# Optimization experiments

Hardware: AMD Instinct MI355X
Metric: run time of the kernel (lower is better)

Reference implementation:

```python
import jax, jax.numpy as jnp
import numpy as np

B, T, D, H = 1, 2048, 1024, 16
HS = D // H  # 64
FF = 4 * D   # 4096
EPS = 1e-6


def rmsnorm(x, w):
    xf = x.astype(jnp.float32)
    n = xf * jax.lax.rsqrt(jnp.mean(xf * xf, axis=-1, keepdims=True) + EPS)
    return n.astype(x.dtype) * w


def setup_inputs() -> dict:
    key = jax.random.key(0)
    ks = jax.random.split(key, 9)
    s = 0.02
    return {
        "x": jax.random.normal(ks[0], (B, T, D), jnp.float32),
        "Wq": jax.random.normal(ks[1], (H, D, HS), jnp.float32) * s,
        "Wk": jax.random.normal(ks[2], (H, D, HS), jnp.float32) * s,
        "Wv": jax.random.normal(ks[3], (H, D, HS), jnp.float32) * s,
        "Wproj": jax.random.normal(ks[4], (H * HS, D), jnp.float32) * s,
        "bproj": jnp.zeros((D,), jnp.float32),
        "W1": jax.random.normal(ks[5], (D, FF), jnp.float32) * s,
        "W2": jax.random.normal(ks[6], (FF, D), jnp.float32) * s,
        "g1": jnp.ones((D,), jnp.float32),
        "g2": jnp.ones((D,), jnp.float32),
    }


def reference(x, Wq, Wk, Wv, Wproj, bproj, W1, W2, g1, g2):
    # --- self attention on RMSNorm(x) ---
    xn = rmsnorm(x, g1)                                   # [B,T,D]
    q = jnp.einsum('btd,hds->bhts', xn, Wq)               # [B,H,T,hs]
    k = jnp.einsum('btd,hds->bhts', xn, Wk)
    v = jnp.einsum('btd,hds->bhts', xn, Wv)
    scale = HS ** -0.5
    wei = jnp.einsum('bhts,bhus->bhtu', q, k) * scale     # [B,H,T,T]
    causal = jnp.tril(jnp.ones((T, T), bool))
    wei = jnp.where(causal, wei, -jnp.inf)
    wei = jax.nn.softmax(wei, axis=-1)
    attn = jnp.einsum('bhtu,bhus->bhts', wei, v)          # [B,H,T,hs]
    attn = attn.transpose(0, 2, 1, 3).reshape(B, T, H * HS)
    sa = attn @ Wproj + bproj                             # [B,T,D]
    x = x + sa
    # --- SiLU FFN on RMSNorm(x) ---
    xn2 = rmsnorm(x, g2)
    h = jax.nn.silu(xn2 @ W1)                             # [B,T,4D]
    x = x + h @ W2
    return x
```

## Files before the change

### kernel.cpp

```cpp
#include <hip/hip_runtime.h>

typedef unsigned short u16;
typedef unsigned int u32;
typedef __attribute__((ext_vector_type(4))) float f32x4;
typedef __attribute__((ext_vector_type(8))) __bf16 bf16x8;

#define T_SEQ 2048
#define DMODEL 1024
#define NHEAD 16
#define HEADS 64
#define FFDIM 4096
#define MNQ 2097152l

__device__ __forceinline__ u16 f2bf(float f) {
  u32 u = __builtin_bit_cast(u32, f);
  u = u + 0x7FFFu + ((u >> 16) & 1u);
  return (u16)(u >> 16);
}
__device__ __forceinline__ float bf2f(u16 h) {
  u32 u = ((u32)h) << 16;
  return __builtin_bit_cast(float, u);
}
__device__ __forceinline__ void gload_lds16(const u16* g, u16* l) {
  __builtin_amdgcn_global_load_lds(
      (const __attribute__((address_space(1))) u32*)g,
      (__attribute__((address_space(3))) u32*)l, 16, 0, 0);
}

__global__ __launch_bounds__(256) void prep_k(
    const float* __restrict__ Wq, const float* __restrict__ Wk,
    const float* __restrict__ Wv, const float* __restrict__ Wproj,
    const float* __restrict__ W1, const float* __restrict__ W2,
    const float* __restrict__ x, const float* __restrict__ g1,
    u16* __restrict__ QKVwT, u16* __restrict__ WprojT,
    u16* __restrict__ W1T, u16* __restrict__ W2T, u16* __restrict__ xn1) {
  __shared__ u16 tile[64 * 66];
  __shared__ float wsum[4];
  int bid = blockIdx.x;
  int tid = threadIdx.x;
  if (bid >= 3072) {
    int row = bid - 3072;
    const float4* xr = (const float4*)(x + (long)row * DMODEL);
    float4 v = xr[tid];
    float ss = v.x * v.x + v.y * v.y + v.z * v.z + v.w * v.w;
#pragma unroll
    for (int off = 32; off >= 1; off >>= 1) ss += __shfl_xor(ss, off, 64);
    if ((tid & 63) == 0) wsum[tid >> 6] = ss;
    __syncthreads();
    float tot = wsum[0] + wsum[1] + wsum[2] + wsum[3];
    float rms = rsqrtf(tot * (1.0f / DMODEL) + 1e-6f);
    float4 gv = ((const float4*)g1)[tid];
    ushort4 o4 = make_ushort4(f2bf(v.x * rms * gv.x), f2bf(v.y * rms * gv.y),
                              f2bf(v.z * rms * gv.z), f2bf(v.w * rms * gv.w));
    ((ushort4*)(xn1 + (long)row * DMODEL))[tid] = o4;
    return;
  }
  const float* in;
  u16* out;
  long ldin, ldout;
  int r0, c0;
  if (bid < 768) {
    int z = bid >> 4, xi = bid & 15;
    int wsel = z >> 4, h = z & 15;
    in = (wsel == 0 ? Wq : (wsel == 1 ? Wk : Wv)) + (long)h * 65536;
    out = QKVwT + (long)wsel * 1048576 + (long)h * 65536;
    ldin = 64; ldout = 1024;
    r0 = xi * 64; c0 = 0;
  } else if (bid < 1024) {
    int b = bid - 768;
    in = Wproj; out = WprojT; ldin = 1024; ldout = 1024;
    r0 = (b >> 4) * 64; c0 = (b & 15) * 64;
  } else if (bid < 2048) {
    int b = bid - 1024;
    in = W1; out = W1T; ldin = 4096; ldout = 1024;
    r0 = (b & 15) * 64; c0 = (b >> 4) * 64;
  } else {
    int b = bid - 2048;
    in = W2; out = W2T; ldin = 1024; ldout = 4096;
    r0 = (b >> 4) * 64; c0 = (b & 15) * 64;
  }
#pragma unroll
  for (int p = 0; p < 16; ++p) {
    int idx = p * 256 + tid;
    int r = idx >> 6, c = idx & 63;
    tile[c * 66 + r] = f2bf(in[(long)(r0 + r) * ldin + c0 + c]);
  }
  __syncthreads();
#pragma unroll
  for (int p = 0; p < 16; ++p) {
    int idx = p * 256 + tid;
    int c = idx >> 6, r = idx & 63;
    out[(long)(c0 + c) * ldout + r0 + r] = tile[c * 66 + r];
  }
}

__global__ __launch_bounds__(256) void proj_rms_k(
    const u16* __restrict__ part, const float* __restrict__ bias,
    const float* __restrict__ resid, const float* __restrict__ g,
    float* __restrict__ x1, u16* __restrict__ xn2) {
  int row = blockIdx.x;
  int tid = threadIdx.x;
  long i = (long)row * DMODEL + tid * 4;
  float4 r = *(const float4*)(resid + i);
  float4 bi = *(const float4*)(bias + tid * 4);
  float4 v;
  v.x = r.x + bi.x; v.y = r.y + bi.y; v.z = r.z + bi.z; v.w = r.w + bi.w;
#pragma unroll
  for (int z = 0; z < 2; ++z) {
    ushort4 a = *(const ushort4*)(part + z * MNQ + i);
    v.x += bf2f(a.x); v.y += bf2f(a.y); v.z += bf2f(a.z); v.w += bf2f(a.w);
  }
  *(float4*)(x1 + i) = v;
  float ss = v.x * v.x + v.y * v.y + v.z * v.z + v.w * v.w;
#pragma unroll
  for (int off = 32; off >= 1; off >>= 1) ss += __shfl_xor(ss, off, 64);
  __shared__ float wsum[4];
  if ((tid & 63) == 0) wsum[tid >> 6] = ss;
  __syncthreads();
  float tot = wsum[0] + wsum[1] + wsum[2] + wsum[3];
  float rms = rsqrtf(tot * (1.0f / DMODEL) + 1e-6f);
  float4 gv = ((const float4*)g)[tid];
  ushort4 o4 = make_ushort4(f2bf(v.x * rms * gv.x), f2bf(v.y * rms * gv.y),
                            f2bf(v.z * rms * gv.z), f2bf(v.w * rms * gv.w));
  ((ushort4*)(xn2 + (long)row * DMODEL))[tid] = o4;
}

template <int EPI, int MODE>
__global__ __launch_bounds__(256, 3) void gemm_bt_k(
    const u16* __restrict__ A, const u16* __restrict__ Bt, int N, int K, int kc,
    u16* __restrict__ out16, u16* __restrict__ vt, u16* __restrict__ part) {
  __shared__ __align__(16) u16 As[3][128 * 32];
  __shared__ __align__(16) u16 Bs[3][128 * 32];
  int tid = threadIdx.x;
  int w = tid >> 6, lane = tid & 63;
  int quad = lane >> 4, l15 = lane & 15;
  int wr = w >> 1, wc = w & 1;

  int bid = blockIdx.x;
  int xcd = bid & 7, s = bid >> 3;
  int nn = N >> 7;
  int bx, by, kz;
  if (MODE == 0) {
    int nl = nn >> 3;
    by = xcd * nl + s % nl;
    int r = s / nl;
    bx = r & 15;
    kz = r >> 4;
  } else {
    bx = xcd * 2 + (s & 1);
    int r = s >> 1;
    by = r % nn;
    kz = r / nn;
  }
  int m0 = bx * 128, n0 = by * 128;

  f32x4 acc[4][4] = {};

  int lr = lane >> 2, lc = (lane & 3) * 8;
  const u16* Ak = A + (long)(m0 + w * 32 + lr) * K + lc + (long)kz * kc;
  const u16* A2k = Ak + (long)16 * K;
  const u16* Bk = Bt + (long)(n0 + w * 32 + lr) * K + lc + (long)kz * kc;
  const u16* B2k = Bk + (long)16 * K;
  u16* Aw[3] = {As[0] + w * 1024, As[1] + w * 1024, As[2] + w * 1024};
  u16* Bw[3] = {Bs[0] + w * 1024, Bs[1] + w * 1024, Bs[2] + w * 1024};

  int niter = kc >> 5;

  gload_lds16(Ak, Aw[0]);
  gload_lds16(A2k, Aw[0] + 512);
  gload_lds16(Bk, Bw[0]);
  gload_lds16(B2k, Bw[0] + 512);
  gload_lds16(Ak + 32, Aw[1]);
  gload_lds16(A2k + 32, Aw[1] + 512);
  gload_lds16(Bk + 32, Bw[1]);
  gload_lds16(B2k + 32, Bw[1] + 512);

  int cb = 0;
  for (int k = 0; k < niter; ++k) {
    if (k + 2 < niter) {
      asm volatile("s_waitcnt vmcnt(4)\n\ts_barrier" ::: "memory");
      int pb = (cb == 0) ? 2 : cb - 1;
      int off = (k + 2) * 32;
      gload_lds16(Ak + off, Aw[pb]);
      gload_lds16(A2k + off, Aw[pb] + 512);
      gload_lds16(Bk + off, Bw[pb]);
      gload_lds16(B2k + off, Bw[pb] + 512);
    } else {
      asm volatile("s_waitcnt vmcnt(0)\n\ts_barrier" ::: "memory");
    }
    const u16* Ab = As[cb];
    const u16* Bb = Bs[cb];
    bf16x8 af[4], bfr[4];
#pragma unroll
    for (int mt = 0; mt < 4; ++mt)
      af[mt] = *(const bf16x8*)(Ab + (wr * 64 + mt * 16 + l15) * 32 + quad * 8);
#pragma unroll
    for (int nt = 0; nt < 4; ++nt)
      bfr[nt] = *(const bf16x8*)(Bb + (wc * 64 + nt * 16 + l15) * 32 + quad * 8);
#pragma unroll
    for (int mt = 0; mt < 4; ++mt)
#pragma unroll
      for (int nt = 0; nt < 4; ++nt)
        acc[mt][nt] = __builtin_amdgcn_mfma_f32_16x16x32_bf16(
            af[mt], bfr[nt], acc[mt][nt], 0, 0, 0);
    cb = (cb == 2) ? 0 : cb + 1;
  }

  bool vblock = (EPI == 0) && (vt != nullptr) && (n0 >= 2048);
  u16* pb = nullptr;
  if (EPI == 4) pb = part + (long)kz * MNQ;
#pragma unroll
  for (int mt = 0; mt < 4; ++mt)
#pragma unroll
    for (int nt = 0; nt < 4; ++nt) {
      int col = n0 + wc * 64 + nt * 16 + l15;
      if (EPI == 0 && vblock) {
        int sc = col - 2048;
        int row0 = m0 + wr * 64 + mt * 16 + quad * 4;
        ushort4 pk = make_ushort4(f2bf(acc[mt][nt][0]), f2bf(acc[mt][nt][1]),
                                  f2bf(acc[mt][nt][2]), f2bf(acc[mt][nt][3]));
        *(ushort4*)(vt + (long)sc * 2048 + row0) = pk;
        continue;
      }
#pragma unroll
      for (int r = 0; r < 4; ++r) {
        int row = m0 + wr * 64 + mt * 16 + quad * 4 + r;
        long idx = (long)row * N + col;
        float v = acc[mt][nt][r];
        if (EPI == 0) {
          out16[idx] = f2bf(v);
        } else if (EPI == 2) {
          out16[idx] = f2bf(v / (1.0f + __expf(-v)));
        } else if (EPI == 4) {
          pb[idx] = f2bf(v);
        }
      }
    }
}

__global__ __launch_bounds__(256) void reduce_ffn2_k(
    const u16* __restrict__ part, const float* __restrict__ resid,
    float* __restrict__ out) {
  long i = ((long)blockIdx.x * 256 + threadIdx.x) * 4;
  float4 r = *(const float4*)(resid + i);
  float4 o = r;
#pragma unroll
  for (int z = 0; z < 4; ++z) {
    ushort4 a = *(const ushort4*)(part + z * MNQ + i);
    o.x += bf2f(a.x); o.y += bf2f(a.y); o.z += bf2f(a.z); o.w += bf2f(a.w);
  }
  *(float4*)(out + i) = o;
}

#define LSTR 72
__global__ __launch_bounds__(256) void attn_part_k(const u16* __restrict__ QKV,
                                                   const u16* __restrict__ Vt,
                                                   u16* __restrict__ Opart,
                                                   float* __restrict__ lpart) {
  __shared__ __align__(16) u16 Qs[64 * LSTR];
  __shared__ __align__(16) u16 Ks[64 * LSTR];
  __shared__ __align__(16) u16 Vs[64 * LSTR];
  __shared__ float lbuf[64];

  int tid = threadIdx.x;
  int w = tid >> 6, lane = tid & 63;
  int quad = lane >> 4, l15 = lane & 15;

  int bid = blockIdx.x;
  int xcd = bid & 7, sg = bid >> 3;
  int h = xcd * 2 + (sg & 1);
  int p = sg >> 1;

  int bx = 0, acc0 = 0;
  while (true) {
    int n = (bx >> 3) + 1;
    if (p < acc0 + n) break;
    acc0 += n;
    ++bx;
  }
  int c = p - acc0;
  int t0 = bx * 64;
  int jstart = c * 8;
  int jend = min(jstart + 8, bx + 1);

#pragma unroll
  for (int pp = 0; pp < 2; ++pp) {
    int idx = pp * 256 + tid;
    int row = idx >> 3, cc = idx & 7;
    *(uint4*)(Qs + row * LSTR + cc * 8) =
        *(const uint4*)(QKV + (long)(t0 + row) * 3072 + h * 64 + cc * 8);
  }
  __syncthreads();
  bf16x8 aq[2];
#pragma unroll
  for (int ks = 0; ks < 2; ++ks)
    aq[ks] = *(const bf16x8*)(Qs + (w * 16 + l15) * LSTR + ks * 32 + quad * 8);

  f32x4 oacc[4] = {};
  float lsum = 0.f;
  int qg = t0 + w * 16 + l15;

  u16* PsW = Qs + w * (16 * LSTR);

  for (int j = jstart; j < jend; ++j) {
    __syncthreads();
#pragma unroll
    for (int pp = 0; pp < 2; ++pp) {
      int idx = pp * 256 + tid;
      int row = idx >> 3, cc = idx & 7;
      *(uint4*)(Ks + row * LSTR + cc * 8) =
          *(const uint4*)(QKV + (long)(j * 64 + row) * 3072 + 1024 + h * 64 + cc * 8);
      *(uint4*)(Vs + row * LSTR + cc * 8) =
          *(const uint4*)(Vt + (long)h * (64 * 2048) + (long)row * 2048 + j * 64 + cc * 8);
    }
    __syncthreads();

    f32x4 sacc[4] = {};
#pragma unroll
    for (int ks = 0; ks < 2; ++ks)
#pragma unroll
      for (int ut = 0; ut < 4; ++ut) {
        bf16x8 kf = *(const bf16x8*)(Ks + (ut * 16 + l15) * LSTR + ks * 32 + quad * 8);
        sacc[ut] = __builtin_amdgcn_mfma_f32_16x16x32_bf16(kf, aq[ks], sacc[ut], 0, 0, 0);
      }

    bool boundary = (j == bx);
#pragma unroll
    for (int ut = 0; ut < 4; ++ut) {
      float pv[4];
#pragma unroll
      for (int r = 0; r < 4; ++r) {
        float v = exp2f(sacc[ut][r] * 0.18033688f);
        if (boundary) {
          int u = j * 64 + ut * 16 + quad * 4 + r;
          if (u > qg) v = 0.f;
        }
        pv[r] = v;
        lsum += v;
      }
      ushort4 pk = make_ushort4(f2bf(pv[0]), f2bf(pv[1]), f2bf(pv[2]), f2bf(pv[3]));
      *(ushort4*)(PsW + l15 * LSTR + ut * 16 + quad * 4) = pk;
    }
    asm volatile("s_waitcnt lgkmcnt(0)" ::: "memory");
#pragma unroll
    for (int ks = 0; ks < 2; ++ks) {
      bf16x8 pf = *(const bf16x8*)(PsW + l15 * LSTR + ks * 32 + quad * 8);
#pragma unroll
      for (int ct = 0; ct < 4; ++ct) {
        bf16x8 vf = *(const bf16x8*)(Vs + (ct * 16 + l15) * LSTR + ks * 32 + quad * 8);
        oacc[ct] = __builtin_amdgcn_mfma_f32_16x16x32_bf16(pf, vf, oacc[ct], 0, 0, 0);
      }
    }
  }

  lsum += __shfl_xor(lsum, 16, 64);
  lsum += __shfl_xor(lsum, 32, 64);
  if (quad == 0) lbuf[w * 16 + l15] = 1.0f / lsum;
  asm volatile("s_waitcnt lgkmcnt(0)" ::: "memory");

  long slot = (long)p * 16 + h;
  float inv[4];
#pragma unroll
  for (int r = 0; r < 4; ++r) inv[r] = lbuf[w * 16 + quad * 4 + r];
  u16* Ob = Opart + slot * 4096;
#pragma unroll
  for (int ct = 0; ct < 4; ++ct)
#pragma unroll
    for (int r = 0; r < 4; ++r)
      Ob[(w * 16 + quad * 4 + r) * 64 + ct * 16 + l15] = f2bf(oacc[ct][r] * inv[r]);
  if (quad == 0) lpart[slot * 64 + w * 16 + l15] = lsum;
}

__global__ __launch_bounds__(256) void attn_combine_k(
    const u16* __restrict__ Opart, const float* __restrict__ lpart,
    u16* __restrict__ out) {
  int bx = blockIdx.x, h = blockIdx.y;
  int g = bx >> 3;
  int p0 = 4 * g * (g + 1) + (bx - 8 * g) * (g + 1);
  int nc = g + 1;
  int tid = threadIdx.x;
  int row = tid >> 2, c4 = (tid & 3) * 16;

  float lv[4];
  float wsum = 0.f;
  for (int cidx = 0; cidx < nc; ++cidx) {
    long slot = (long)(p0 + cidx) * 16 + h;
    lv[cidx] = lpart[slot * 64 + row];
    wsum += lv[cidx];
  }
  float rinv = 1.0f / wsum;

  float o[16];
#pragma unroll
  for (int i = 0; i < 16; ++i) o[i] = 0.f;
  for (int cidx = 0; cidx < nc; ++cidx) {
    float wc = lv[cidx] * rinv;
    const u16* Ob = Opart + ((long)(p0 + cidx) * 16 + h) * 4096 + row * 64 + c4;
    bf16x8 a = *(const bf16x8*)Ob;
    bf16x8 b = *(const bf16x8*)(Ob + 8);
#pragma unroll
    for (int i = 0; i < 8; ++i) {
      o[i] += wc * (float)a[i];
      o[8 + i] += wc * (float)b[i];
    }
  }
  u16 ob[16];
#pragma unroll
  for (int i = 0; i < 16; ++i) ob[i] = f2bf(o[i]);
  u16* op = out + (long)(bx * 64 + row) * 1024 + h * 64 + c4;
  *(uint4*)op = *(uint4*)ob;
  *(uint4*)(op + 8) = *(uint4*)(ob + 8);
}

extern "C" void kernel_launch(void* const* d_in, const int* in_sizes, int n_in,
                              void* d_out, int out_size, void* d_ws, size_t ws_size,
                              hipStream_t stream) {
  const float* x     = (const float*)d_in[0];
  const float* Wq    = (const float*)d_in[1];
  const float* Wk    = (const float*)d_in[2];
  const float* Wv    = (const float*)d_in[3];
  const float* Wproj = (const float*)d_in[4];
  const float* bproj = (const float*)d_in[5];
  const float* W1    = (const float*)d_in[6];
  const float* W2    = (const float*)d_in[7];
  const float* g1    = (const float*)d_in[8];
  const float* g2    = (const float*)d_in[9];

  char* ws = (char*)d_ws;
  u16* QKVwT  = (u16*)(ws);
  u16* WprojT = (u16*)(ws + (6ul << 20));
  u16* W1T    = (u16*)(ws + (8ul << 20));
  u16* W2T    = (u16*)(ws + (16ul << 20));
  u16* xn1    = (u16*)(ws + (24ul << 20));
  u16* QKVb   = (u16*)(ws + (28ul << 20));
  u16* VtB    = (u16*)(ws + (40ul << 20));
  u16* attn   = (u16*)(ws + (44ul << 20));
  float* x1   = (float*)(ws + (48ul << 20));
  u16* xn2    = (u16*)(ws + (56ul << 20));
  u16* hbuf   = (u16*)(ws + (60ul << 20));
  u16* Opart    = (u16*)(ws + (48ul << 20));
  float* lpart  = (float*)(ws + (58ul << 20));
  u16* projp    = (u16*)(ws + (28ul << 20));
  u16* ffn2p    = (u16*)(ws + (28ul << 20));
  if (ws_size < (76ul << 20)) return;

  dim3 blk(256);

  prep_k<<<dim3(5120), blk, 0, stream>>>(
      Wq, Wk, Wv, Wproj, W1, W2, x, g1, QKVwT, WprojT, W1T, W2T, xn1);
  gemm_bt_k<0, 0><<<dim3(384), blk, 0, stream>>>(
      xn1, QKVwT, 3072, 1024, 1024, QKVb, VtB, nullptr);
  attn_part_k<<<dim3(1280), blk, 0, stream>>>(QKVb, VtB, Opart, lpart);
  attn_combine_k<<<dim3(32, 16), blk, 0, stream>>>(Opart, lpart, attn);
  gemm_bt_k<4, 0><<<dim3(256), blk, 0, stream>>>(
      attn, WprojT, 1024, 1024, 512, nullptr, nullptr, projp);
  proj_rms_k<<<dim3(2048), blk, 0, stream>>>(projp, bproj, x, g2, x1, xn2);
  gemm_bt_k<2, 0><<<dim3(512), blk, 0, stream>>>(
      xn2, W1T, 4096, 1024, 1024, hbuf, nullptr, nullptr);
  gemm_bt_k<4, 1><<<dim3(512), blk, 0, stream>>>(
      hbuf, W2T, 1024, 4096, 1024, nullptr, nullptr, ffn2p);
  reduce_ffn2_k<<<dim3(2048), blk, 0, stream>>>(ffn2p, x1, (float*)d_out);
}
```

Baseline: 254.9 us.

## Template GEMM K-loop count, split FFN2 over 8 K chunks, write single-chunk attention directly

The GEMM kernel now takes its iteration count as a template parameter so the K loop fully unrolls and buffer indices become compile-time constants. The FFN2 GEMM is split over eight K chunks instead of four, doubling the grid to 1024 blocks, with partials written to two buffers and summed in the reduce kernel. Attention blocks for the first query tiles, which have only one KV chunk, now write normalized output straight into the attention buffer, and the combine kernel skips those tiles. The cost is more partial-sum traffic for FFN2 and larger unrolled code.

```diff
diff --git a/kernel.cpp b/kernel.cpp
--- a/kernel.cpp
+++ b/kernel.cpp
@@ -125,12 +125,15 @@
   ((ushort4*)(xn2 + (long)row * DMODEL))[tid] = o4;
 }
 
-template <int EPI, int MODE>
+template <int EPI, int MODE, int NITER>
 __global__ __launch_bounds__(256, 3) void gemm_bt_k(
-    const u16* __restrict__ A, const u16* __restrict__ Bt, int N, int K, int kc,
-    u16* __restrict__ out16, u16* __restrict__ vt, u16* __restrict__ part) {
+    const u16* __restrict__ A, const u16* __restrict__ Bt, int N,
+    u16* __restrict__ out16, u16* __restrict__ vt,
+    u16* __restrict__ p0, u16* __restrict__ p1) {
   __shared__ __align__(16) u16 As[3][128 * 32];
   __shared__ __align__(16) u16 Bs[3][128 * 32];
+  const int K = 1024 * ((EPI == 4 && MODE == 1) ? 4 : 1);
+  const int kc = NITER * 32;
   int tid = threadIdx.x;
   int w = tid >> 6, lane = tid & 63;
   int quad = lane >> 4, l15 = lane & 15;
@@ -161,30 +164,27 @@
   const u16* A2k = Ak + (long)16 * K;
   const u16* Bk = Bt + (long)(n0 + w * 32 + lr) * K + lc + (long)kz * kc;
   const u16* B2k = Bk + (long)16 * K;
-  u16* Aw[3] = {As[0] + w * 1024, As[1] + w * 1024, As[2] + w * 1024};
-  u16* Bw[3] = {Bs[0] + w * 1024, Bs[1] + w * 1024, Bs[2] + w * 1024};
-
-  int niter = kc >> 5;
-
-  gload_lds16(Ak, Aw[0]);
-  gload_lds16(A2k, Aw[0] + 512);
-  gload_lds16(Bk, Bw[0]);
-  gload_lds16(B2k, Bw[0] + 512);
-  gload_lds16(Ak + 32, Aw[1]);
-  gload_lds16(A2k + 32, Aw[1] + 512);
-  gload_lds16(Bk + 32, Bw[1]);
-  gload_lds16(B2k + 32, Bw[1] + 512);
-
-  int cb = 0;
-  for (int k = 0; k < niter; ++k) {
-    if (k + 2 < niter) {
+
+  gload_lds16(Ak, As[0] + w * 1024);
+  gload_lds16(A2k, As[0] + w * 1024 + 512);
+  gload_lds16(Bk, Bs[0] + w * 1024);
+  gload_lds16(B2k, Bs[0] + w * 1024 + 512);
+  gload_lds16(Ak + 32, As[1] + w * 1024);
+  gload_lds16(A2k + 32, As[1] + w * 1024 + 512);
+  gload_lds16(Bk + 32, Bs[1] + w * 1024);
+  gload_lds16(B2k + 32, Bs[1] + w * 1024 + 512);
+
+#pragma unroll
+  for (int k = 0; k < NITER; ++k) {
+    const int cb = k % 3;
+    if (k + 2 < NITER) {
       asm volatile("s_waitcnt vmcnt(4)\n\ts_barrier" ::: "memory");
-      int pb = (cb == 0) ? 2 : cb - 1;
-      int off = (k + 2) * 32;
-      gload_lds16(Ak + off, Aw[pb]);
-      gload_lds16(A2k + off, Aw[pb] + 512);
-      gload_lds16(Bk + off, Bw[pb]);
-      gload_lds16(B2k + off, Bw[pb] + 512);
+      const int pb = (k + 2) % 3;
+      const int off = (k + 2) * 32;
+      gload_lds16(Ak + off, As[pb] + w * 1024);
+      gload_lds16(A2k + off, As[pb] + w * 1024 + 512);
+      gload_lds16(Bk + off, Bs[pb] + w * 1024);
+      gload_lds16(B2k + off, Bs[pb] + w * 1024 + 512);
     } else {
       asm volatile("s_waitcnt vmcnt(0)\n\ts_barrier" ::: "memory");
     }
@@ -203,12 +203,11 @@
       for (int nt = 0; nt < 4; ++nt)
         acc[mt][nt] = __builtin_amdgcn_mfma_f32_16x16x32_bf16(
             af[mt], bfr[nt], acc[mt][nt], 0, 0, 0);
-    cb = (cb == 2) ? 0 : cb + 1;
   }
 
   bool vblock = (EPI == 0) && (vt != nullptr) && (n0 >= 2048);
   u16* pb = nullptr;
-  if (EPI == 4) pb = part + (long)kz * MNQ;
+  if (EPI == 4) pb = (kz < 4 ? p0 : p1) + (long)(kz & 3) * MNQ;
 #pragma unroll
   for (int mt = 0; mt < 4; ++mt)
 #pragma unroll
@@ -239,15 +238,19 @@
 }
 
 __global__ __launch_bounds__(256) void reduce_ffn2_k(
-    const u16* __restrict__ part, const float* __restrict__ resid,
-    float* __restrict__ out) {
+    const u16* __restrict__ p0, const u16* __restrict__ p1,
+    const float* __restrict__ resid, float* __restrict__ out) {
   long i = ((long)blockIdx.x * 256 + threadIdx.x) * 4;
   float4 r = *(const float4*)(resid + i);
   float4 o = r;
 #pragma unroll
   for (int z = 0; z < 4; ++z) {
-    ushort4 a = *(const ushort4*)(part + z * MNQ + i);
-    o.x += bf2f(a.x); o.y += bf2f(a.y); o.z += bf2f(a.z); o.w += bf2f(a.w);
+    ushort4 a = *(const ushort4*)(p0 + z * MNQ + i);
+    ushort4 b = *(const ushort4*)(p1 + z * MNQ + i);
+    o.x += bf2f(a.x) + bf2f(b.x);
+    o.y += bf2f(a.y) + bf2f(b.y);
+    o.z += bf2f(a.z) + bf2f(b.z);
+    o.w += bf2f(a.w) + bf2f(b.w);
   }
   *(float4*)(out + i) = o;
 }
@@ -256,7 +259,8 @@
 __global__ __launch_bounds__(256) void attn_part_k(const u16* __restrict__ QKV,
                                                    const u16* __restrict__ Vt,
                                                    u16* __restrict__ Opart,
-                                                   float* __restrict__ lpart) {
+                                                   float* __restrict__ lpart,
+                                                   u16* __restrict__ attn) {
   __shared__ __align__(16) u16 Qs[64 * LSTR];
   __shared__ __align__(16) u16 Ks[64 * LSTR];
   __shared__ __align__(16) u16 Vs[64 * LSTR];
@@ -358,10 +362,20 @@
   if (quad == 0) lbuf[w * 16 + l15] = 1.0f / lsum;
   asm volatile("s_waitcnt lgkmcnt(0)" ::: "memory");
 
+  float inv[4];
+#pragma unroll
+  for (int r = 0; r < 4; ++r) inv[r] = lbuf[w * 16 + quad * 4 + r];
+
+  if (bx < 8) {
+#pragma unroll
+    for (int ct = 0; ct < 4; ++ct)
+#pragma unroll
+      for (int r = 0; r < 4; ++r)
+        attn[(long)(t0 + w * 16 + quad * 4 + r) * 1024 + h * 64 + ct * 16 + l15] =
+            f2bf(oacc[ct][r] * inv[r]);
+    return;
+  }
   long slot = (long)p * 16 + h;
-  float inv[4];
-#pragma unroll
-  for (int r = 0; r < 4; ++r) inv[r] = lbuf[w * 16 + quad * 4 + r];
   u16* Ob = Opart + slot * 4096;
 #pragma unroll
   for (int ct = 0; ct < 4; ++ct)
@@ -374,7 +388,7 @@
 __global__ __launch_bounds__(256) void attn_combine_k(
     const u16* __restrict__ Opart, const float* __restrict__ lpart,
     u16* __restrict__ out) {
-  int bx = blockIdx.x, h = blockIdx.y;
+  int bx = blockIdx.x + 8, h = blockIdx.y;
   int g = bx >> 3;
   int p0 = 4 * g * (g + 1) + (bx - 8 * g) * (g + 1);
   int nc = g + 1;
@@ -441,23 +455,24 @@
   u16* Opart    = (u16*)(ws + (48ul << 20));
   float* lpart  = (float*)(ws + (58ul << 20));
   u16* projp    = (u16*)(ws + (28ul << 20));
-  u16* ffn2p    = (u16*)(ws + (28ul << 20));
+  u16* ffn2pA   = (u16*)(ws + (28ul << 20));
+  u16* ffn2pB   = (u16*)(ws);
   if (ws_size < (76ul << 20)) return;
 
   dim3 blk(256);
 
   prep_k<<<dim3(5120), blk, 0, stream>>>(
       Wq, Wk, Wv, Wproj, W1, W2, x, g1, QKVwT, WprojT, W1T, W2T, xn1);
-  gemm_bt_k<0, 0><<<dim3(384), blk, 0, stream>>>(
-      xn1, QKVwT, 3072, 1024, 1024, QKVb, VtB, nullptr);
-  attn_part_k<<<dim3(1280), blk, 0, stream>>>(QKVb, VtB, Opart, lpart);
-  attn_combine_k<<<dim3(32, 16), blk, 0, stream>>>(Opart, lpart, attn);
-  gemm_bt_k<4, 0><<<dim3(256), blk, 0, stream>>>(
-      attn, WprojT, 1024, 1024, 512, nullptr, nullptr, projp);
+  gemm_bt_k<0, 0, 32><<<dim3(384), blk, 0, stream>>>(
+      xn1, QKVwT, 3072, QKVb, VtB, nullptr, nullptr);
+  attn_part_k<<<dim3(1280), blk, 0, stream>>>(QKVb, VtB, Opart, lpart, attn);
+  attn_combine_k<<<dim3(24, 16), blk, 0, stream>>>(Opart, lpart, attn);
+  gemm_bt_k<4, 0, 16><<<dim3(256), blk, 0, stream>>>(
+      attn, WprojT, 1024, nullptr, nullptr, projp, nullptr);
   proj_rms_k<<<dim3(2048), blk, 0, stream>>>(projp, bproj, x, g2, x1, xn2);
-  gemm_bt_k<2, 0><<<dim3(512), blk, 0, stream>>>(
-      xn2, W1T, 4096, 1024, 1024, hbuf, nullptr, nullptr);
-  gemm_bt_k<4, 1><<<dim3(512), blk, 0, stream>>>(
-      hbuf, W2T, 1024, 4096, 1024, nullptr, nullptr, ffn2p);
-  reduce_ffn2_k<<<dim3(2048), blk, 0, stream>>>(ffn2p, x1, (float*)d_out);
-}
+  gemm_bt_k<2, 0, 32><<<dim3(512), blk, 0, stream>>>(
+      xn2, W1T, 4096, hbuf, nullptr, nullptr, nullptr);
+  gemm_bt_k<4, 1, 16><<<dim3(1024), blk, 0, stream>>>(
+      hbuf, W2T, 1024, nullptr, nullptr, ffn2pA, ffn2pB);
+  reduce_ffn2_k<<<dim3(2048), blk, 0, stream>>>(ffn2pA, ffn2pB, x1, (float*)d_out);
+}
```

Measured after the change: 246.9 us. 1.03x faster.
